# Kernel optimization log

Measured on AMD Instinct MI355X. Metric: run time of the kernel, lower is better.

## Reference

```python
import jax, jax.numpy as jnp
import numpy as np

TAU = 2.0
THR = 1.0
ALPHA = 10.0
FLOW_SCALE = 16.0  # 2 ** flow_scale_pow2 (=4)
DECAY = 1.0 - 1.0 / TAU


def conv2d(x, w, b=None, stride=1, pad=0):
    # x: [N,C,H,W], w: [O,I,kh,kw]
    out = jax.lax.conv_general_dilated(
        x, w, (stride, stride), [(pad, pad), (pad, pad)],
        dimension_numbers=('NCHW', 'OIHW', 'NCHW'))
    if b is not None:
        out = out + b[None, :, None, None]
    return out


@jax.custom_vjp
def spike(v):
    return (v > 0).astype(v.dtype)

def _spike_fwd(v):
    return (v > 0).astype(v.dtype), v

def _spike_bwd(v, g):
    s = jax.nn.sigmoid(ALPHA * v)
    return (g * ALPHA * s * (1.0 - s),)

spike.defvjp(_spike_fwd, _spike_bwd)


def lif(x, w, b, mem, stride, pad):
    """Conv + leaky-integrate-fire with soft reset. mem init 0 -> first step mem=cur."""
    cur = conv2d(x, w, b, stride, pad)
    mem = mem * DECAY + cur
    s = spike(mem - THR)
    mem = mem - s * THR
    return s, mem


def up2(x):
    return jnp.repeat(jnp.repeat(x, 2, axis=2), 2, axis=3)


def forward(x, w_e1, b_e1, w_e2, b_e2, w_e3, b_e3, w_d3, b_d3,
            w_d2, b_d2, w_d1, b_d1, w_skip2, w_skip1, w_flow, b_flow):
    N, T, C, H, W = x.shape
    bc = w_e1.shape[0]  # base_ch = 32
    z = lambda c, h, w: jnp.zeros((N, c, h, w), x.dtype)
    init = (
        z(bc, H // 2, W // 2),      # mem_e1
        z(2 * bc, H // 4, W // 4),  # mem_e2
        z(4 * bc, H // 8, W // 8),  # mem_e3
        z(2 * bc, H // 4, W // 4),  # mem_d3
        z(bc, H // 2, W // 2),      # mem_d2
        z(bc, H, W),                # mem_d1
        z(bc, H // 2, W // 2),      # mean_e1 (zeros + /(t+1) rule == None-init)
        z(2 * bc, H // 4, W // 4),  # mean_e2
        z(2, H, W),                 # flow_mean
    )

    def step(carry, inp):
        t, xt = inp
        m1, m2, m3, md3, md2, md1, me1, me2, fm = carry
        s1, m1 = lif(xt, w_e1, b_e1, m1, 2, 2)
        s2, m2 = lif(s1, w_e2, b_e2, m2, 2, 1)
        s3, m3 = lif(s2, w_e3, b_e3, m3, 2, 1)
        tf = (t + 1).astype(xt.dtype)
        me1 = me1 + (s1 - me1) / tf
        me2 = me2 + (s2 - me2) / tf
        d3, md3 = lif(up2(s3), w_d3, b_d3, md3, 1, 1)
        d3 = d3 + conv2d(me2, w_skip2)
        d2, md2 = lif(up2(d3), w_d2, b_d2, md2, 1, 1)
        d2 = d2 + conv2d(me1, w_skip1)
        d1, md1 = lif(up2(d2), w_d1, b_d1, md1, 1, 1)
        flow = conv2d(d1, w_flow, b_flow, 1, 1) * FLOW_SCALE
        fm = fm + (flow - fm) / tf
        return (m1, m2, m3, md3, md2, md1, me1, me2, fm), flow

    _, flows = jax.lax.scan(step, init, (jnp.arange(T), jnp.moveaxis(x, 1, 0)))
    return flows[-1]  # return_last_flow=True -> flow of final timestep [N,2,H,W]


def setup_inputs() -> dict:
    key = jax.random.key(0)
    ks = jax.random.split(key, 16)
    N, T, H, W, bc = 4, 8, 256, 256, 32

    def w(k, o, i, kh, kw):
        return jax.random.normal(k, (o, i, kh, kw), jnp.float32) / np.sqrt(i * kh * kw)

    return {
        'x': jax.random.uniform(ks[0], (N, T, 2, H, W), jnp.float32),
        'w_e1': w(ks[1], bc, 2, 5, 5), 'b_e1': jnp.zeros((bc,), jnp.float32),
        'w_e2': w(ks[2], 2 * bc, bc, 3, 3), 'b_e2': jnp.zeros((2 * bc,), jnp.float32),
        'w_e3': w(ks[3], 4 * bc, 2 * bc, 3, 3), 'b_e3': jnp.zeros((4 * bc,), jnp.float32),
        'w_d3': w(ks[4], 2 * bc, 4 * bc, 3, 3), 'b_d3': jnp.zeros((2 * bc,), jnp.float32),
        'w_d2': w(ks[5], bc, 2 * bc, 3, 3), 'b_d2': jnp.zeros((bc,), jnp.float32),
        'w_d1': w(ks[6], bc, bc, 3, 3), 'b_d1': jnp.zeros((bc,), jnp.float32),
        'w_skip2': w(ks[7], 2 * bc, 2 * bc, 1, 1),
        'w_skip1': w(ks[8], bc, bc, 1, 1),
        'w_flow': w(ks[9], 2, bc, 3, 3), 'b_flow': jnp.zeros((2,), jnp.float32),
    }


def reference(x, w_e1, b_e1, w_e2, b_e2, w_e3, b_e3, w_d3, b_d3,
              w_d2, b_d2, w_d1, b_d1, w_skip2, w_skip1, w_flow, b_flow):
    return forward(x, w_e1, b_e1, w_e2, b_e2, w_e3, b_e3, w_d3, b_d3,
                   w_d2, b_d2, w_d1, b_d1, w_skip2, w_skip1, w_flow, b_flow)
```

## Files before the change

### kernel.cpp

```cpp
#include <hip/hip_runtime.h>
#include <cstdint>
#include <cstddef>


static constexpr float THRc   = 1.0f;
static constexpr float DECAYc = 0.5f;

__device__ __forceinline__ float getc(const float4& v, int k) {
    switch (k & 3) {
        case 0: return v.x;
        case 1: return v.y;
        case 2: return v.z;
        default: return v.w;
    }
}

__global__ __launch_bounds__(256) void prep_collapse(const float* __restrict__ w,
                                                     float* __restrict__ wc, int pairs)
{
    int idx = blockIdx.x * 256 + threadIdx.x;
    if (idx >= pairs) return;
    float a[3][3];
#pragma unroll
    for (int i = 0; i < 3; ++i)
#pragma unroll
        for (int j = 0; j < 3; ++j) a[i][j] = w[idx * 9 + i * 3 + j];
    float rs[2][2][3];
#pragma unroll
    for (int kx = 0; kx < 3; ++kx) {
        rs[0][0][kx] = a[0][kx];
        rs[0][1][kx] = a[1][kx] + a[2][kx];
        rs[1][0][kx] = a[0][kx] + a[1][kx];
        rs[1][1][kx] = a[2][kx];
    }
#pragma unroll
    for (int py = 0; py < 2; ++py)
#pragma unroll
        for (int px = 0; px < 2; ++px)
#pragma unroll
            for (int r = 0; r < 2; ++r) {
                float c0, c1;
                if (px == 0) { c0 = rs[py][r][0];               c1 = rs[py][r][1] + rs[py][r][2]; }
                else         { c0 = rs[py][r][0] + rs[py][r][1]; c1 = rs[py][r][2]; }
                wc[idx * 16 + ((py * 2 + px) * 2 + r) * 2 + 0] = c0;
                wc[idx * 16 + ((py * 2 + px) * 2 + r) * 2 + 1] = c1;
            }
}

template<int IC, int ICC, int OC, int SIH, int SIW, int CPT, int YPB, int OCT,
         int NW, int SKIP_IC, int SKC>
__global__ __launch_bounds__(NW * 64) void dec_conv(
    const float* __restrict__ in,
    const float* __restrict__ wc,
    const float* __restrict__ bias,
    float* __restrict__ mem,
    float* __restrict__ out,
    const float* __restrict__ skip_in,
    const float* __restrict__ skip_w)
{
    constexpr int NT   = NW * 64;
    constexpr int LPT  = SIW / CPT;
    static_assert((CPT & 1) == 0 && (CPT == 2 || (CPT & 3) == 0), "CPT even (2 or mult of 4)");
    static_assert(LPT * YPB == 64, "wave must tile the band");
    static_assert((ICC & 1) == 0, "ICC even for wA/wB ping-pong");
    constexpr int OC_B = NW * OCT;
    constexpr int NOCB = OC / OC_B;
    constexpr int NYB  = SIH / YPB;
    constexpr int SP   = SIW + 8;
    constexpr int SR   = YPB + 2;
    constexpr int OH   = 2 * SIH, OW = 2 * SIW;
    constexpr int NCH  = IC / ICC;
    constexpr int W4   = SIW / 4;
    constexpr int TILE = ICC * SR * SP;
    constexpr int OROWS = 2 * YPB;
    constexpr int SKTILE = (SKIP_IC > 0) ? SKC * OROWS * OW : 0;
    constexpr int BASE = TILE > SKTILE ? TILE : SKTILE;

    __shared__ __align__(16) float sb[BASE];

    int b = blockIdx.x;
    const int ocb = b % NOCB; b /= NOCB;
    const int yb  = b % NYB;  b /= NYB;
    const int n   = b;
    const int y0  = yb * YPB;

    const int lane = threadIdx.x & 63;
    const int wav  = threadIdx.x >> 6;
    const int cl   = lane % LPT;
    const int yp   = lane / LPT;
    const int c0   = cl * CPT;
    const int y    = y0 + yp;

    const int oc0 = __builtin_amdgcn_readfirstlane(ocb * OC_B + wav * OCT);

    int lzero;
    asm volatile("v_mov_b32 %0, 0" : "=v"(lzero));
    const float4* wlane = reinterpret_cast<const float4*>(wc) + lzero;
    const int wbase = oc0 * IC * 4;

    for (int f = threadIdx.x; f < ICC * SR * 2; f += NT) {
        int side = f & 1;
        int t    = f >> 1;
        int r    = t % SR;
        int ic   = t / SR;
        sb[(ic * SR + r) * SP + (side ? (SIW + 4) : 3)] = 0.0f;
    }

    float acc[OCT][2][2 * CPT];
#pragma unroll
    for (int j = 0; j < OCT; ++j) {
        float bv = bias[oc0 + j];
#pragma unroll
        for (int py = 0; py < 2; ++py)
#pragma unroll
            for (int q = 0; q < 2 * CPT; ++q) acc[j][py][q] = bv;
    }

    const float* inn = in + (size_t)n * IC * SIH * SIW;

    float4 wA[OCT * 4], wB[OCT * 4];
    auto wload = [&](int icg, float4* dst) {
#pragma unroll
        for (int j = 0; j < OCT; ++j)
#pragma unroll
            for (int g = 0; g < 4; ++g)
                dst[j * 4 + g] = wlane[wbase + (j * IC + icg) * 4 + g];
    };

    auto compute = [&](int icl, const float4* w) {
        float s[3][CPT + 2];
#pragma unroll
        for (int r = 0; r < 3; ++r) {
            const int rb = (icl * SR + yp + r) * SP;
            s[r][0] = sb[rb + 3 + c0];
            if constexpr (CPT >= 4) {
#pragma unroll
                for (int v = 0; v < CPT / 4; ++v) {
                    float4 t4 = *reinterpret_cast<const float4*>(&sb[rb + 4 + c0 + 4 * v]);
                    s[r][1 + 4 * v] = t4.x; s[r][2 + 4 * v] = t4.y;
                    s[r][3 + 4 * v] = t4.z; s[r][4 + 4 * v] = t4.w;
                }
            } else {
                float2 t2 = *reinterpret_cast<const float2*>(&sb[rb + 4 + c0]);
                s[r][1] = t2.x; s[r][2] = t2.y;
            }
            s[r][CPT + 1] = sb[rb + 4 + c0 + CPT];
        }
#pragma unroll
        for (int j = 0; j < OCT; ++j)
#pragma unroll
            for (int py = 0; py < 2; ++py)
#pragma unroll
                for (int cc = 0; cc < CPT; ++cc)
#pragma unroll
                    for (int px = 0; px < 2; ++px) {
                        float v = acc[j][py][cc * 2 + px];
#pragma unroll
                        for (int rr = 0; rr < 2; ++rr)
#pragma unroll
                            for (int c2 = 0; c2 < 2; ++c2)
                                v += getc(w[j * 4 + py * 2 + px], rr * 2 + c2)
                                   * s[py + rr][cc + px + c2];
                        acc[j][py][cc * 2 + px] = v;
                    }
    };

    wload(0, wA);
    for (int ch = 0; ch < NCH; ++ch) {
        __syncthreads();
        const float* inb = inn + (size_t)ch * ICC * SIH * SIW;
        constexpr int SLOTS = ICC * SR * W4;
        for (int f = threadIdx.x; f < SLOTS; f += NT) {
            int c4 = f & (W4 - 1);
            int t  = f / W4;
            int r  = t % SR;
            int ic = t / SR;
            int sy = y0 - 1 + r;
            float4 v = make_float4(0.f, 0.f, 0.f, 0.f);
            if (sy >= 0 && sy < SIH)
                v = *reinterpret_cast<const float4*>(
                        inb + (size_t)ic * SIH * SIW + (size_t)sy * SIW + 4 * c4);
            *reinterpret_cast<float4*>(&sb[(ic * SR + r) * SP + 4 + 4 * c4]) = v;
        }
        __syncthreads();
        const int icg0 = ch * ICC;
        for (int ic = 0; ic < ICC; ic += 2) {
            wload(icg0 + ic + 1, wB);
            compute(ic, wA);
            wload(icg0 + ic + 2, wA);
            compute(ic + 1, wB);
        }
    }

    constexpr int NV = (2 * CPT) / 4;
    float sk[OCT][2][2 * CPT] = {};
    if constexpr (SKIP_IC > 0) {
        constexpr int NSK = SKIP_IC / SKC;
        constexpr int OW4 = OW / 4;
        const float* skn = skip_in + (size_t)n * SKIP_IC * OH * OW;
        for (int sc = 0; sc < NSK; ++sc) {
            __syncthreads();
            for (int f = threadIdx.x; f < SKC * OROWS * OW4; f += NT) {
                int c4 = f & (OW4 - 1);
                int t  = f / OW4;
                int r  = t % OROWS;
                int ic = t / OROWS;
                *reinterpret_cast<float4*>(&sb[(ic * OROWS + r) * OW + 4 * c4]) =
                    *reinterpret_cast<const float4*>(
                        skn + ((size_t)(sc * SKC + ic) * OH + 2 * y0 + r) * OW + 4 * c4);
            }
            __syncthreads();
            float wsk[OCT][SKC];
#pragma unroll
            for (int j = 0; j < OCT; ++j)
#pragma unroll
                for (int ic = 0; ic < SKC; ++ic)
                    wsk[j][ic] = skip_w[(size_t)(oc0 + j) * SKIP_IC + sc * SKC + ic];
#pragma unroll
            for (int ic = 0; ic < SKC; ++ic)
#pragma unroll
                for (int py = 0; py < 2; ++py)
#pragma unroll
                    for (int v = 0; v < NV; ++v) {
                        float4 sv = *reinterpret_cast<const float4*>(
                            &sb[(ic * OROWS + 2 * yp + py) * OW + 2 * c0 + 4 * v]);
#pragma unroll
                        for (int j = 0; j < OCT; ++j) {
                            sk[j][py][4 * v + 0] += wsk[j][ic] * sv.x;
                            sk[j][py][4 * v + 1] += wsk[j][ic] * sv.y;
                            sk[j][py][4 * v + 2] += wsk[j][ic] * sv.z;
                            sk[j][py][4 * v + 3] += wsk[j][ic] * sv.w;
                        }
                    }
        }
    }

    const bool wout = (out != nullptr);
#pragma unroll
    for (int j = 0; j < OCT; ++j)
#pragma unroll
        for (int py = 0; py < 2; ++py) {
            size_t ob = (((size_t)n * OC + oc0 + j) * OH + (2 * y + py)) * OW + 2 * c0;
#pragma unroll
            for (int v = 0; v < NV; ++v) {
                float4 mv = *reinterpret_cast<const float4*>(&mem[ob + 4 * v]);
                float4 ov, nm;
                float m0 = mv.x * DECAYc + acc[j][py][4 * v + 0];
                float m1 = mv.y * DECAYc + acc[j][py][4 * v + 1];
                float m2 = mv.z * DECAYc + acc[j][py][4 * v + 2];
                float m3 = mv.w * DECAYc + acc[j][py][4 * v + 3];
                float s0 = (m0 - THRc) > 0.0f ? 1.0f : 0.0f;
                float s1 = (m1 - THRc) > 0.0f ? 1.0f : 0.0f;
                float s2 = (m2 - THRc) > 0.0f ? 1.0f : 0.0f;
                float s3 = (m3 - THRc) > 0.0f ? 1.0f : 0.0f;
                nm.x = m0 - s0 * THRc; nm.y = m1 - s1 * THRc;
                nm.z = m2 - s2 * THRc; nm.w = m3 - s3 * THRc;
                *reinterpret_cast<float4*>(&mem[ob + 4 * v]) = nm;
                if (wout) {
                    ov.x = s0 + sk[j][py][4 * v + 0];
                    ov.y = s1 + sk[j][py][4 * v + 1];
                    ov.z = s2 + sk[j][py][4 * v + 2];
                    ov.w = s3 + sk[j][py][4 * v + 3];
                    *reinterpret_cast<float4*>(&out[ob + 4 * v]) = ov;
                }
            }
        }
}

template<int IC, int ICC, int OC, int IH, int IW, int K, int CPT, int LPT, int OCT, bool DO_MEAN>
__global__ __launch_bounds__(256) void enc_conv(
    const float* __restrict__ in, int in_nstride,
    const float* __restrict__ wgt,
    const float* __restrict__ bias,
    float* __restrict__ mem,
    float* __restrict__ out,
    float* __restrict__ mean,
    float inv_tf)
{
    constexpr int P    = K / 2;
    constexpr int OH   = IH / 2, OW = IW / 2;
    constexpr int SPr  = 4 + IW + P;
    constexpr int SP   = (SPr + 3) & ~3;
    constexpr int OC_B = 4 * OCT;
    constexpr int NOCB = OC / OC_B;
    constexpr int RL   = 2 * CPT + 2 * P - 1;
    constexpr int NCH  = IC / ICC;
    constexpr int W4   = IW / 4;
    static_assert(LPT * CPT == OW, "lanes x CPT must cover OW");
    static_assert((ICC & (ICC - 1)) == 0, "ICC pow2");

    __shared__ float sb[K][ICC][SP];

    int b = blockIdx.x;
    const int ocb = b % NOCB; b /= NOCB;
    const int y   = b % OH;   b /= OH;
    const int n   = b;

    const int lane = threadIdx.x & 63;
    const int wav  = threadIdx.x >> 6;
    const int x0   = (lane % LPT) * CPT;
    const int oc0  = __builtin_amdgcn_readfirstlane(ocb * OC_B + wav * OCT);

    for (int f = threadIdx.x; f < K * ICC * 2 * P; f += 256) {
        int h  = f % (2 * P);
        int t  = f / (2 * P);
        int ic = t & (ICC - 1);
        int r  = t / ICC;
        int col = (h < P) ? (4 - P + h) : (4 + IW + h - P);
        sb[r][ic][col] = 0.0f;
    }

    float acc[OCT][CPT];
#pragma unroll
    for (int j = 0; j < OCT; ++j) {
        float bv = bias[oc0 + j];
#pragma unroll
        for (int cc = 0; cc < CPT; ++cc) acc[j][cc] = bv;
    }

    const float* inn = in + (size_t)n * (size_t)in_nstride;

    for (int ch = 0; ch < NCH; ++ch) {
        __syncthreads();
        const float* inb = inn + (size_t)ch * ICC * IH * IW;
        constexpr int SLOTS = K * ICC * W4;
        for (int f = threadIdx.x; f < SLOTS; f += 256) {
            int c4 = f & (W4 - 1);
            int t  = f / W4;
            int ic = t & (ICC - 1);
            int r  = t / ICC;
            int sy = 2 * y - P + r;
            float4 v = make_float4(0.f, 0.f, 0.f, 0.f);
            if (sy >= 0 && sy < IH)
                v = *reinterpret_cast<const float4*>(
                        inb + (size_t)ic * IH * IW + (size_t)sy * IW + 4 * c4);
            *reinterpret_cast<float4*>(&sb[r][ic][4 + 4 * c4]) = v;
        }
        __syncthreads();
        for (int ic = 0; ic < ICC; ++ic) {
            float s[K][RL];
#pragma unroll
            for (int r = 0; r < K; ++r)
#pragma unroll
                for (int k = 0; k < RL; ++k)
                    s[r][k] = sb[r][ic][4 - P + 2 * x0 + k];
            const float* wp = wgt + ((size_t)oc0 * IC + ch * ICC + ic) * (K * K);
#pragma unroll
            for (int j = 0; j < OCT; ++j) {
                float wv[K * K];
#pragma unroll
                for (int k = 0; k < K * K; ++k) wv[k] = wp[(size_t)j * IC * K * K + k];
#pragma unroll
                for (int cc = 0; cc < CPT; ++cc)
#pragma unroll
                    for (int ky = 0; ky < K; ++ky)
#pragma unroll
                        for (int kx = 0; kx < K; ++kx)
                            acc[j][cc] += wv[ky * K + kx] * s[ky][2 * cc + kx];
            }
        }
    }

    if (lane < LPT) {
#pragma unroll
        for (int j = 0; j < OCT; ++j) {
            size_t ob = (((size_t)n * OC + oc0 + j) * OH + y) * OW + x0;
#pragma unroll
            for (int cc = 0; cc < CPT; ++cc) {
                float m  = mem[ob + cc] * DECAYc + acc[j][cc];
                float sp = (m - THRc) > 0.0f ? 1.0f : 0.0f;
                mem[ob + cc] = m - sp * THRc;
                if constexpr (DO_MEAN) {
                    float mv = mean[ob + cc];
                    mean[ob + cc] = mv + (sp - mv) * inv_tf;
                }
                out[ob + cc] = sp;
            }
        }
    }
}

template<int IC, int OC, int IH, int IW, int OH, int OW,
         int K, int STRIDE, int PAD, bool UP2, int SKIP_IC,
         bool DO_LIF, bool DO_MEAN>
__global__ __launch_bounds__(256) void conv_fused(
    const float* __restrict__ in, int in_nstride,
    const float* __restrict__ wgt,
    const float* __restrict__ bias,
    float* __restrict__ mem,
    float* __restrict__ out,
    const float* __restrict__ skip_in,
    const float* __restrict__ skip_w,
    float* __restrict__ mean,
    float inv_tf, float outscale)
{
    constexpr int VEC  = 4;
    constexpr int OWV  = OW / VEC;
    constexpr int WSZ  = IC * K * K;
    constexpr int SIH  = UP2 ? IH / 2 : IH;
    constexpr int SIW  = UP2 ? IW / 2 : IW;
    constexpr int RLEN = (VEC - 1) * STRIDE + K;

    __shared__ float sw[WSZ];

    const int bstart = blockIdx.x * 256;
    const int oc = (bstart / (OH * OWV)) % OC;

    for (int i = threadIdx.x; i < WSZ; i += 256) sw[i] = wgt[oc * WSZ + i];
    __syncthreads();

    const int idx = bstart + threadIdx.x;
    const int wx  = idx % OWV;
    int tt        = idx / OWV;
    const int oy  = tt % OH; tt /= OH;
    tt /= OC;
    const int n   = tt;
    const int ox0 = wx * VEC;

    const float bv = bias ? bias[oc] : 0.0f;
    float acc[VEC];
#pragma unroll
    for (int v = 0; v < VEC; ++v) acc[v] = bv;

    const float* inn = in + (size_t)n * (size_t)in_nstride;

    for (int ic = 0; ic < IC; ++ic) {
        const float* inc = inn + (size_t)ic * (SIH * SIW);
#pragma unroll
        for (int ky = 0; ky < K; ++ky) {
            const int uy = oy * STRIDE + ky - PAD;
            const bool rowok = (uy >= 0) & (uy < IH);
            int sy = UP2 ? (uy >> 1) : uy;
            sy = sy < 0 ? 0 : (sy > SIH - 1 ? SIH - 1 : sy);
            const float* __restrict__ row = inc + (size_t)sy * SIW;

            float r[RLEN];
#pragma unroll
            for (int j = 0; j < RLEN; ++j) {
                const int ux = ox0 * STRIDE - PAD + j;
                const bool ok = rowok & (ux >= 0) & (ux < IW);
                int sx = UP2 ? (ux >> 1) : ux;
                sx = sx < 0 ? 0 : (sx > SIW - 1 ? SIW - 1 : sx);
                r[j] = ok ? row[sx] : 0.0f;
            }
#pragma unroll
            for (int kx = 0; kx < K; ++kx) {
                const float wv = sw[(ic * K + ky) * K + kx];
#pragma unroll
                for (int v = 0; v < VEC; ++v)
                    acc[v] += r[v * STRIDE + kx] * wv;
            }
        }
    }

    const size_t obase = ((((size_t)n * OC + oc) * OH) + oy) * (size_t)OW + ox0;
#pragma unroll
    for (int v = 0; v < VEC; ++v) out[obase + v] = acc[v] * outscale;
}

extern "C" void kernel_launch(void* const* d_in, const int* in_sizes, int n_in,
                              void* d_out, int out_size, void* d_ws, size_t ws_size,
                              hipStream_t stream)
{
    const float* x     = (const float*)d_in[0];
    const float* w_e1  = (const float*)d_in[1];
    const float* b_e1  = (const float*)d_in[2];
    const float* w_e2  = (const float*)d_in[3];
    const float* b_e2  = (const float*)d_in[4];
    const float* w_e3  = (const float*)d_in[5];
    const float* b_e3  = (const float*)d_in[6];
    const float* w_d3  = (const float*)d_in[7];
    const float* b_d3  = (const float*)d_in[8];
    const float* w_d2  = (const float*)d_in[9];
    const float* b_d2  = (const float*)d_in[10];
    const float* w_d1  = (const float*)d_in[11];
    const float* b_d1  = (const float*)d_in[12];
    const float* w_sk2 = (const float*)d_in[13];
    const float* w_sk1 = (const float*)d_in[14];
    const float* w_fl  = (const float*)d_in[15];
    const float* b_fl  = (const float*)d_in[16];
    float* outp = (float*)d_out;

    float* ws = (float*)d_ws;
    size_t off = 0;
    auto alloc = [&](size_t nelem) { float* p = ws + off; off += nelem; return p; };

    float* m1  = alloc(4UL * 32 * 128 * 128);
    float* m2  = alloc(4UL * 64 * 64 * 64);
    float* m3  = alloc(4UL * 128 * 32 * 32);
    float* md3 = alloc(4UL * 64 * 64 * 64);
    float* md2 = alloc(4UL * 32 * 128 * 128);
    float* md1 = alloc(4UL * 32 * 256 * 256);
    float* me1 = alloc(4UL * 32 * 128 * 128);
    float* me2 = alloc(4UL * 64 * 64 * 64);
    const size_t zcount = off;
    float* s1  = alloc(4UL * 32 * 128 * 128);
    float* s2  = alloc(4UL * 64 * 64 * 64);
    float* s3  = alloc(4UL * 128 * 32 * 32);
    float* d3a = alloc(4UL * 64 * 64 * 64);
    float* d2a = alloc(4UL * 32 * 128 * 128);
    float* d1a = alloc(4UL * 32 * 256 * 256);
    float* wc3 = alloc(64UL * 128 * 16 + 64);
    float* wc2 = alloc(32UL * 64 * 16 + 64);
    float* wc1 = alloc(32UL * 32 * 16 + 64);
    (void)ws_size; (void)in_sizes; (void)n_in; (void)out_size;

    hipMemsetAsync(d_ws, 0, zcount * sizeof(float), stream);

    prep_collapse<<<(64 * 128 + 255) / 256, 256, 0, stream>>>(w_d3, wc3, 64 * 128);
    prep_collapse<<<(32 * 64 + 255) / 256, 256, 0, stream>>>(w_d2, wc2, 32 * 64);
    prep_collapse<<<(32 * 32 + 255) / 256, 256, 0, stream>>>(w_d1, wc1, 32 * 32);

    for (int t = 0; t < 8; ++t) {
        const float inv_tf = 1.0f / (float)(t + 1);
        const float* xt = x + (size_t)t * 2 * 256 * 256;

        enc_conv<2, 2, 32, 256, 256, 5, 2, 64, 2, true>
            <<<4 * 128 * 4, 256, 0, stream>>>(xt, 8 * 2 * 256 * 256, w_e1, b_e1,
                                              m1, s1, me1, inv_tf);
        enc_conv<32, 16, 64, 128, 128, 3, 1, 64, 2, true>
            <<<4 * 64 * 8, 256, 0, stream>>>(s1, 32 * 128 * 128, w_e2, b_e2,
                                             m2, s2, me2, inv_tf);
        enc_conv<64, 32, 128, 64, 64, 3, 1, 32, 4, false>
            <<<4 * 32 * 8, 256, 0, stream>>>(s2, 64 * 64 * 64, w_e3, b_e3,
                                             m3, s3, nullptr, inv_tf);
        dec_conv<128, 32, 64, 32, 32, 2, 4, 1, 4, 64, 8>
            <<<4 * 8 * 16, 256, 0, stream>>>(s3, wc3, b_d3, md3, d3a, me2, w_sk2);
        dec_conv<64, 16, 32, 64, 64, 2, 2, 2, 4, 32, 8>
            <<<4 * 32 * 4, 256, 0, stream>>>(d3a, wc2, b_d2, md2, d2a, me1, w_sk1);
        dec_conv<32, 8, 32, 128, 128, 8, 4, 1, 4, 0, 1>
            <<<4 * 32 * 8, 256, 0, stream>>>(d2a, wc1, b_d1, md1,
                                             (t == 7) ? d1a : nullptr, nullptr, nullptr);
        if (t == 7) {
            conv_fused<32, 2, 256, 256, 256, 256, 3, 1, 1, false, 0, false, false>
                <<<512, 256, 0, stream>>>(d1a, 32 * 256 * 256, w_fl, b_fl,
                                          nullptr, outp, nullptr, nullptr, nullptr, inv_tf, 16.0f);
        }
    }
}
```

Measured before the change: 2.403 ms.

## Double-buffer input tiles in dec_conv and retune decoder tile shapes

The decoder conv kernel now keeps two shared-memory input tiles. It stages the next channel chunk while computing on the current one, which removes one barrier per chunk and hides global-load latency. The template parameters for the d3 and d1 decoder launches change: ICC drops to 16 for d3, and d1 switches to a smaller-band tiling with more blocks. The cost is twice the shared-memory tile size, which may reduce occupancy.

```diff
diff --git a/kernel.cpp b/kernel.cpp
--- a/kernel.cpp
+++ b/kernel.cpp
@@ -74,7 +74,8 @@
     constexpr int TILE = ICC * SR * SP;
     constexpr int OROWS = 2 * YPB;
     constexpr int SKTILE = (SKIP_IC > 0) ? SKC * OROWS * OW : 0;
-    constexpr int BASE = TILE > SKTILE ? TILE : SKTILE;
+    constexpr int BASE = (2 * TILE) > SKTILE ? (2 * TILE) : SKTILE;
+    constexpr int SLOTS = ICC * SR * W4;
 
     __shared__ __align__(16) float sb[BASE];
 
@@ -98,12 +99,14 @@
     const float4* wlane = reinterpret_cast<const float4*>(wc) + lzero;
     const int wbase = oc0 * IC * 4;
 
-    for (int f = threadIdx.x; f < ICC * SR * 2; f += NT) {
+    for (int f = threadIdx.x; f < 2 * ICC * SR * 2; f += NT) {
         int side = f & 1;
         int t    = f >> 1;
         int r    = t % SR;
-        int ic   = t / SR;
-        sb[(ic * SR + r) * SP + (side ? (SIW + 4) : 3)] = 0.0f;
+        int tt   = t / SR;
+        int ic   = tt % ICC;
+        int buf  = tt / ICC;
+        sb[buf * TILE + (ic * SR + r) * SP + (side ? (SIW + 4) : 3)] = 0.0f;
     }
 
     float acc[OCT][2][2 * CPT];
@@ -127,49 +130,9 @@
                 dst[j * 4 + g] = wlane[wbase + (j * IC + icg) * 4 + g];
     };
 
-    auto compute = [&](int icl, const float4* w) {
-        float s[3][CPT + 2];
-#pragma unroll
-        for (int r = 0; r < 3; ++r) {
-            const int rb = (icl * SR + yp + r) * SP;
-            s[r][0] = sb[rb + 3 + c0];
-            if constexpr (CPT >= 4) {
-#pragma unroll
-                for (int v = 0; v < CPT / 4; ++v) {
-                    float4 t4 = *reinterpret_cast<const float4*>(&sb[rb + 4 + c0 + 4 * v]);
-                    s[r][1 + 4 * v] = t4.x; s[r][2 + 4 * v] = t4.y;
-                    s[r][3 + 4 * v] = t4.z; s[r][4 + 4 * v] = t4.w;
-                }
-            } else {
-                float2 t2 = *reinterpret_cast<const float2*>(&sb[rb + 4 + c0]);
-                s[r][1] = t2.x; s[r][2] = t2.y;
-            }
-            s[r][CPT + 1] = sb[rb + 4 + c0 + CPT];
-        }
-#pragma unroll
-        for (int j = 0; j < OCT; ++j)
-#pragma unroll
-            for (int py = 0; py < 2; ++py)
-#pragma unroll
-                for (int cc = 0; cc < CPT; ++cc)
-#pragma unroll
-                    for (int px = 0; px < 2; ++px) {
-                        float v = acc[j][py][cc * 2 + px];
-#pragma unroll
-                        for (int rr = 0; rr < 2; ++rr)
-#pragma unroll
-                            for (int c2 = 0; c2 < 2; ++c2)
-                                v += getc(w[j * 4 + py * 2 + px], rr * 2 + c2)
-                                   * s[py + rr][cc + px + c2];
-                        acc[j][py][cc * 2 + px] = v;
-                    }
-    };
-
-    wload(0, wA);
-    for (int ch = 0; ch < NCH; ++ch) {
-        __syncthreads();
+    auto stage = [&](int buf, int ch) {
         const float* inb = inn + (size_t)ch * ICC * SIH * SIW;
-        constexpr int SLOTS = ICC * SR * W4;
+        float* dst = sb + buf * TILE;
         for (int f = threadIdx.x; f < SLOTS; f += NT) {
             int c4 = f & (W4 - 1);
             int t  = f / W4;
@@ -180,16 +143,62 @@
             if (sy >= 0 && sy < SIH)
                 v = *reinterpret_cast<const float4*>(
                         inb + (size_t)ic * SIH * SIW + (size_t)sy * SIW + 4 * c4);
-            *reinterpret_cast<float4*>(&sb[(ic * SR + r) * SP + 4 + 4 * c4]) = v;
-        }
-        __syncthreads();
+            *reinterpret_cast<float4*>(&dst[(ic * SR + r) * SP + 4 + 4 * c4]) = v;
+        }
+    };
+
+    auto compute = [&](const float* bp, int icl, const float4* w) {
+        float s[3][CPT + 2];
+#pragma unroll
+        for (int r = 0; r < 3; ++r) {
+            const int rb = (icl * SR + yp + r) * SP;
+            s[r][0] = bp[rb + 3 + c0];
+            if constexpr (CPT >= 4) {
+#pragma unroll
+                for (int v = 0; v < CPT / 4; ++v) {
+                    float4 t4 = *reinterpret_cast<const float4*>(&bp[rb + 4 + c0 + 4 * v]);
+                    s[r][1 + 4 * v] = t4.x; s[r][2 + 4 * v] = t4.y;
+                    s[r][3 + 4 * v] = t4.z; s[r][4 + 4 * v] = t4.w;
+                }
+            } else {
+                float2 t2 = *reinterpret_cast<const float2*>(&bp[rb + 4 + c0]);
+                s[r][1] = t2.x; s[r][2] = t2.y;
+            }
+            s[r][CPT + 1] = bp[rb + 4 + c0 + CPT];
+        }
+#pragma unroll
+        for (int j = 0; j < OCT; ++j)
+#pragma unroll
+            for (int py = 0; py < 2; ++py)
+#pragma unroll
+                for (int cc = 0; cc < CPT; ++cc)
+#pragma unroll
+                    for (int px = 0; px < 2; ++px) {
+                        float v = acc[j][py][cc * 2 + px];
+#pragma unroll
+                        for (int rr = 0; rr < 2; ++rr)
+#pragma unroll
+                            for (int c2 = 0; c2 < 2; ++c2)
+                                v += getc(w[j * 4 + py * 2 + px], rr * 2 + c2)
+                                   * s[py + rr][cc + px + c2];
+                        acc[j][py][cc * 2 + px] = v;
+                    }
+    };
+
+    wload(0, wA);
+    stage(0, 0);
+    __syncthreads();
+    for (int ch = 0; ch < NCH; ++ch) {
+        if (ch + 1 < NCH) stage((ch + 1) & 1, ch + 1);
+        const float* bp = sb + (ch & 1) * TILE;
         const int icg0 = ch * ICC;
         for (int ic = 0; ic < ICC; ic += 2) {
             wload(icg0 + ic + 1, wB);
-            compute(ic, wA);
+            compute(bp, ic, wA);
             wload(icg0 + ic + 2, wA);
-            compute(ic + 1, wB);
-        }
+            compute(bp, ic + 1, wB);
+        }
+        __syncthreads();
     }
 
     constexpr int NV = (2 * CPT) / 4;
@@ -199,7 +208,7 @@
         constexpr int OW4 = OW / 4;
         const float* skn = skip_in + (size_t)n * SKIP_IC * OH * OW;
         for (int sc = 0; sc < NSK; ++sc) {
-            __syncthreads();
+            if (sc) __syncthreads();
             for (int f = threadIdx.x; f < SKC * OROWS * OW4; f += NT) {
                 int c4 = f & (OW4 - 1);
                 int t  = f / OW4;
@@ -524,13 +533,13 @@
         enc_conv<64, 32, 128, 64, 64, 3, 1, 32, 4, false>
             <<<4 * 32 * 8, 256, 0, stream>>>(s2, 64 * 64 * 64, w_e3, b_e3,
                                              m3, s3, nullptr, inv_tf);
-        dec_conv<128, 32, 64, 32, 32, 2, 4, 1, 4, 64, 8>
+        dec_conv<128, 16, 64, 32, 32, 2, 4, 1, 4, 64, 8>
             <<<4 * 8 * 16, 256, 0, stream>>>(s3, wc3, b_d3, md3, d3a, me2, w_sk2);
         dec_conv<64, 16, 32, 64, 64, 2, 2, 2, 4, 32, 8>
             <<<4 * 32 * 4, 256, 0, stream>>>(d3a, wc2, b_d2, md2, d2a, me1, w_sk1);
-        dec_conv<32, 8, 32, 128, 128, 8, 4, 1, 4, 0, 1>
-            <<<4 * 32 * 8, 256, 0, stream>>>(d2a, wc1, b_d1, md1,
-                                             (t == 7) ? d1a : nullptr, nullptr, nullptr);
+        dec_conv<32, 8, 32, 128, 128, 2, 1, 2, 4, 0, 1>
+            <<<4 * 128 * 4, 256, 0, stream>>>(d2a, wc1, b_d1, md1,
+                                              (t == 7) ? d1a : nullptr, nullptr, nullptr);
         if (t == 7) {
             conv_fused<32, 2, 256, 256, 256, 256, 3, 1, 1, false, 0, false, false>
                 <<<512, 256, 0, stream>>>(d1a, 32 * 256 * 256, w_fl, b_fl,
```

Result: faster. 2.225 ms (-7.4%).
